# Kernel tuning notes

Hardware: AMD Instinct MI355X
Metric: run time of the kernel (lower is better)

## Reference

```python
import jax, jax.numpy as jnp
import numpy as np

Q, C, D, H, K, B, T = 10000, 200, 64, 64, 4, 512, 200
MAX_DISC = 10.0


def setup_inputs() -> dict:
    key = jax.random.key(0)
    ks = jax.random.split(key, 24)

    def p(k, shape, s=0.05):
        return jax.random.normal(k, shape, jnp.float32) * s

    mid_qd = (D + C) // 2   # 132
    mid_la = (H + C) // 2   # 132
    mid_dc = (D + 1) // 2   # 32
    inp = {
        'E_q': p(ks[0], (Q + 1, D)),
        'E_c': p(ks[1], (C + 1, D)),
        'E_it': p(ks[2], (101, D)),
        'E_ut': p(ks[3], (101, D)),
        'E_nh': p(ks[4], (101, D)),
        'W_fuse': p(ks[5], (D, 3 * D)), 'b_fuse': jnp.zeros((D,), jnp.float32),
        'W_ih': p(ks[6], (3 * H, 5 * D)), 'b_ih': jnp.zeros((3 * H,), jnp.float32),
        'W_hh': p(ks[7], (3 * H, H)), 'b_hh': jnp.zeros((3 * H,), jnp.float32),
        'qd_W1': p(ks[8], (mid_qd, D)), 'qd_b1': jnp.zeros((mid_qd,), jnp.float32),
        'qd_W2': p(ks[9], (C, mid_qd)), 'qd_b2': jnp.zeros((C,), jnp.float32),
        'la_W1': p(ks[10], (mid_la, H)), 'la_b1': jnp.zeros((mid_la,), jnp.float32),
        'la_W2': p(ks[11], (C, mid_la)), 'la_b2': jnp.zeros((C,), jnp.float32),
        'dc_W1': p(ks[12], (mid_dc, D)), 'dc_b1': jnp.zeros((mid_dc,), jnp.float32),
        'dc_W2': p(ks[13], (1, mid_dc)), 'dc_b2': jnp.zeros((1,), jnp.float32),
    }
    inp['question_seq'] = jax.random.randint(ks[14], (B, T), 0, Q + 1, jnp.int32)
    inp['correct_seq'] = jax.random.randint(ks[15], (B, T), 0, 2, jnp.int32)
    inp['interval_time_seq'] = jax.random.randint(ks[16], (B, T), 0, 101, jnp.int32)
    inp['use_time_seq'] = jax.random.randint(ks[17], (B, T), 0, 101, jnp.int32)
    inp['num_hint_seq'] = jax.random.randint(ks[18], (B, T), 0, 101, jnp.int32)
    inp['num_attempt_seq'] = jax.random.randint(ks[19], (B, T), 0, 101, jnp.int32)
    # per-question concept lists + padding mask (first nc entries valid)
    q2c = jax.random.randint(ks[20], (Q + 1, K), 0, C, jnp.int32)
    nc = jax.random.randint(ks[21], (Q + 1,), 1, K + 1, jnp.int32)
    mask = (jnp.arange(K, dtype=jnp.int32)[None, :] < nc[:, None]).astype(jnp.int32)
    inp['q2c_table'] = q2c
    inp['q2c_mask'] = mask
    rows = jnp.arange(Q + 1)[:, None]
    inp['Q_table'] = jnp.zeros((Q + 1, C), jnp.float32).at[rows, q2c].max(mask.astype(jnp.float32))
    return inp


def mlp2(x, W1, b1, W2, b2):
    # MLP4Proj, num_layer=2, eval-mode dropout == identity
    return jax.nn.relu(x @ W1.T + b1) @ W2.T + b2


def gru(x, W_ih, b_ih, W_hh, b_hh):
    # torch nn.GRU, 1 layer, batch_first; gate order r,z,n
    xp = jnp.einsum('btd,gd->btg', x, W_ih) + b_ih  # [B,T,3H]

    def step(h, xp_t):
        gh = h @ W_hh.T + b_hh
        xr, xz, xn = jnp.split(xp_t, 3, axis=-1)
        hr, hz, hn = jnp.split(gh, 3, axis=-1)
        r = jax.nn.sigmoid(xr + hr)
        z = jax.nn.sigmoid(xz + hz)
        n = jnp.tanh(xn + r * hn)
        h_new = (1.0 - z) * n + z * h
        return h_new, h_new

    h0 = jnp.zeros((x.shape[0], W_hh.shape[1]), x.dtype)
    _, hs = jax.lax.scan(step, h0, jnp.swapaxes(xp, 0, 1))
    return jnp.swapaxes(hs, 0, 1)  # [B,T,H]


def reference(E_q, E_c, E_it, E_ut, E_nh, W_fuse, b_fuse, W_ih, b_ih, W_hh, b_hh,
              qd_W1, qd_b1, qd_W2, qd_b2, la_W1, la_b1, la_W2, la_b2,
              dc_W1, dc_b1, dc_W2, dc_b2, Q_table,
              question_seq, correct_seq, interval_time_seq, use_time_seq,
              num_hint_seq, num_attempt_seq, q2c_table, q2c_mask):
    qe = E_q[question_seq]                                   # [B,T,D]
    # get_concept_emb: difficulty-weighted concept fusion
    qd = jax.nn.sigmoid(mlp2(qe, qd_W1, qd_b1, qd_W2, qd_b2))  # [B,T,C]
    qc_idx = q2c_table[question_seq]                          # [B,T,K]
    msk = q2c_mask[question_seq].astype(qe.dtype)             # [B,T,K]
    rel = jnp.take_along_axis(qd, qc_idx, axis=2) * msk       # [B,T,K]
    srel = rel.sum(-1, keepdims=True) + 1e-6
    ce = (rel[..., None] * E_c[qc_idx]).sum(-2) / srel        # [B,T,D]
    corr = jnp.broadcast_to(correct_seq[..., None].astype(qe.dtype), qe.shape)
    inter = jnp.concatenate([qe, ce, corr], axis=-1)          # [B,T,3D]
    # aux-info fusion (source bug: num_attempt also uses embed_num_hint)
    ut_nh_na = jnp.concatenate([E_ut[use_time_seq], E_nh[num_hint_seq], E_nh[num_attempt_seq]], axis=-1)
    fuse = ut_nh_na @ W_fuse.T + b_fuse                       # [B,T,D]
    x = jnp.concatenate([inter, E_it[interval_time_seq], fuse], axis=-1)  # [B,T,5D]
    latent = gru(x, W_ih, b_ih, W_hh, b_hh)                   # [B,T,H]
    # predict_score on shifted slices
    lat, qe2, qs2 = latent[:, :-1], qe[:, 1:], question_seq[:, 1:]
    ua = jax.nn.sigmoid(mlp2(lat, la_W1, la_b1, la_W2, la_b2))       # [B,T-1,C]
    disc = jax.nn.sigmoid(mlp2(qe2, dc_W1, dc_b1, dc_W2, dc_b2)) * MAX_DISC  # [B,T-1,1]
    qd2 = jax.nn.sigmoid(mlp2(qe2, qd_W1, qd_b1, qd_W2, qd_b2))      # [B,T-1,C]
    Qt = Q_table[qs2]                                                # [B,T-1,C]
    ua_m = ua * Qt
    qd_m = qd2 * Qt
    sw = qd_m.sum(-1, keepdims=True) + 1e-6
    y = disc * (ua_m - qd_m) / sw
    return jax.nn.sigmoid(y.sum(-1))                                 # [B,T-1]
```

## Files before the change

kernel.cpp:

```cpp
#include <hip/hip_runtime.h>
#include <hip/hip_fp16.h>

constexpr int QN  = 10001;
constexpr int BB  = 512;
constexpr int TT  = 200;
constexpr int QPB = 32;

__device__ __forceinline__ float sigm(float x) { return 1.f / (1.f + __expf(-x)); }
__device__ __forceinline__ float tanh_fast(float x) { return 1.f - 2.f / (1.f + __expf(2.f * x)); }

__device__ __forceinline__ unsigned packh_rtne(float lo, float hi) {
    return ((unsigned)__half_as_ushort(__float2half(hi)) << 16) |
            (unsigned)__half_as_ushort(__float2half(lo));
}

typedef _Float16 half2_t __attribute__((ext_vector_type(2)));
typedef float f4v __attribute__((ext_vector_type(4)));
__device__ __forceinline__ half2_t u2h(unsigned u) {
    union { unsigned u; half2_t h; } x; x.u = u; return x.h;
}

#if __has_builtin(__builtin_amdgcn_fdot2)
__device__ __forceinline__ float fdot2u(unsigned wu, unsigned hu, float acc) {
    return __builtin_amdgcn_fdot2(u2h(wu), u2h(hu), acc, false);
}
#else
__device__ __forceinline__ float fdot2u(unsigned wu, unsigned hu, float acc) {
    float wlo = __half2float(__ushort_as_half((unsigned short)(wu & 0xffffu)));
    float whi = __half2float(__ushort_as_half((unsigned short)(wu >> 16)));
    float hlo = __half2float(__ushort_as_half((unsigned short)(hu & 0xffffu)));
    float hhi = __half2float(__ushort_as_half((unsigned short)(hu >> 16)));
    return acc + wlo * hlo + whi * hhi;
}
#endif

__global__ void k_tables(const float* __restrict__ E_c, const float* __restrict__ E_it,
                         const float* __restrict__ E_ut, const float* __restrict__ E_nh,
                         const float* __restrict__ W_fuse, const float* __restrict__ b_fuse,
                         const float* __restrict__ W_ih, const float* __restrict__ b_ih,
                         float* __restrict__ T_c, float* __restrict__ T_it,
                         float* __restrict__ T_ut, float* __restrict__ T_nh, float* __restrict__ T_na,
                         float* __restrict__ bias0, float* __restrict__ Vcorr)
{
    int blk = blockIdx.x, j = threadIdx.x;
    __shared__ float s_e[64];
    __shared__ float s_t[64];
    const int ilv = (j & 63) * 3 + (j >> 6);

    if (blk < 201) {
        if (j < 64) s_e[j] = E_c[blk * 64 + j];
        __syncthreads();
        float a = 0.f;
        #pragma unroll
        for (int k = 0; k < 64; k++) a += W_ih[j * 320 + 64 + k] * s_e[k];
        T_c[blk * 192 + j] = a;
    } else if (blk < 302) {
        int r = blk - 201;
        if (j < 64) s_e[j] = E_it[r * 64 + j];
        __syncthreads();
        float a = 0.f;
        #pragma unroll
        for (int k = 0; k < 64; k++) a += W_ih[j * 320 + 192 + k] * s_e[k];
        T_it[r * 192 + ilv] = a;
    } else if (blk < 605) {
        int which = (blk - 302) / 101;
        int r     = (blk - 302) % 101;
        const float* E = (which == 0) ? E_ut : E_nh;
        int fofs = which * 64;
        if (j < 64) s_e[j] = E[r * 64 + j];
        __syncthreads();
        if (j < 64) {
            float a = 0.f;
            #pragma unroll
            for (int d = 0; d < 64; d++) a += W_fuse[j * 192 + fofs + d] * s_e[d];
            s_t[j] = a;
        }
        __syncthreads();
        float a = 0.f;
        #pragma unroll
        for (int e = 0; e < 64; e++) a += W_ih[j * 320 + 256 + e] * s_t[e];
        float* outp = (which == 0) ? T_ut : ((which == 1) ? T_nh : T_na);
        outp[r * 192 + ilv] = a;
    } else {
        float a = b_ih[j];
        #pragma unroll
        for (int e = 0; e < 64; e++) a += W_ih[j * 320 + 256 + e] * b_fuse[e];
        bias0[j] = a;
        float v = 0.f;
        #pragma unroll
        for (int k = 0; k < 64; k++) v += W_ih[j * 320 + 128 + k];
        Vcorr[j] = v;
    }
}

__global__ void __launch_bounds__(192) k_perq(
    const float* __restrict__ E_q, const float* __restrict__ W_ih,
    const float* __restrict__ qd_W1, const float* __restrict__ qd_b1,
    const float* __restrict__ qd_W2, const float* __restrict__ qd_b2,
    const float* __restrict__ dc_W1, const float* __restrict__ dc_b1,
    const float* __restrict__ dc_W2, const float* __restrict__ dc_b2,
    const int* __restrict__ q2c, const int* __restrict__ q2cm,
    const float* __restrict__ T_c,
    float* __restrict__ Xq, float* __restrict__ disc,
    float* __restrict__ qds, float* __restrict__ wdk)
{
    __shared__ float s_wbuf[192 * 66];
    __shared__ float s_qe[QPB][64];
    __shared__ float s_wq[QPB][4];
    __shared__ int   s_cq[QPB][4];
    __shared__ float s_hidw[3][136];

    const int tid = threadIdx.x, w = tid >> 6, l = tid & 63;
    const int q0 = blockIdx.x * QPB;

    for (int i = tid; i < 132 * 64; i += 192)
        s_wbuf[(i >> 6) * 66 + (i & 63)] = qd_W1[i];
    for (int i = tid; i < 32 * 64; i += 192)
        s_wbuf[(132 + (i >> 6)) * 66 + (i & 63)] = dc_W1[i];
    for (int i = tid; i < QPB * 64; i += 192) {
        int qq = i >> 6, q = q0 + qq;
        s_qe[qq][i & 63] = E_q[(q < QN ? q : 0) * 64 + (i & 63)];
    }
    __syncthreads();

    for (int qq = w; qq < QPB; qq += 3) {
        int q = q0 + qq;
        bool valid = q < QN;
        int qc = valid ? q : 0;
        int cc[4], mm[4];
        #pragma unroll
        for (int k = 0; k < 4; k++) { cc[k] = q2c[qc * 4 + k]; mm[k] = q2cm[qc * 4 + k]; }

        float qe[64];
        #pragma unroll
        for (int k4 = 0; k4 < 16; k4++) {
            float4 v = *(const float4*)(&s_qe[qq][k4 * 4]);
            qe[4 * k4] = v.x; qe[4 * k4 + 1] = v.y; qe[4 * k4 + 2] = v.z; qe[4 * k4 + 3] = v.w;
        }

        auto rowdot = [&](int r) {
            const float* wr = s_wbuf + r * 66;
            float a = 0.f;
            #pragma unroll
            for (int jj = 0; jj < 32; jj++) {
                float2 ww = *(const float2*)(wr + 2 * jj);
                a += ww.x * qe[2 * jj] + ww.y * qe[2 * jj + 1];
            }
            return a;
        };

        s_hidw[w][l]      = fmaxf(rowdot(l)      + qd_b1[l],      0.f);
        s_hidw[w][64 + l] = fmaxf(rowdot(64 + l) + qd_b1[64 + l], 0.f);
        if (l < 4)
            s_hidw[w][128 + l] = fmaxf(rowdot(128 + l) + qd_b1[128 + l], 0.f);
        float dch = 0.f;
        if (l < 32) dch = fmaxf(rowdot(132 + l) + dc_b1[l], 0.f);

        int g = l >> 4, li = l & 15;
        int c = cc[g];
        float acc = 0.f;
        #pragma unroll
        for (int i = 0; i < 9; i++) {
            int m = li + 16 * i;
            if (m < 132) acc += qd_W2[c * 132 + m] * s_hidw[w][m];
        }
        acc += __shfl_xor(acc, 1); acc += __shfl_xor(acc, 2);
        acc += __shfl_xor(acc, 4); acc += __shfl_xor(acc, 8);
        float r0 = __shfl(acc, 0), r1 = __shfl(acc, 16);
        float r2 = __shfl(acc, 32), r3 = __shfl(acc, 48);

        float raw[4] = { sigm(r0 + qd_b2[cc[0]]), sigm(r1 + qd_b2[cc[1]]),
                         sigm(r2 + qd_b2[cc[2]]), sigm(r3 + qd_b2[cc[3]]) };
        float rel[4];
        #pragma unroll
        for (int k = 0; k < 4; k++) rel[k] = raw[k] * (float)mm[k];
        float sr = rel[0] + rel[1] + rel[2] + rel[3] + 1e-6f;

        float qsum = 0.f, wdv[4];
        #pragma unroll
        for (int k = 0; k < 4; k++) {
            float wd = 0.f;
            if (mm[k]) {
                bool dup = false;
                for (int jj = 0; jj < k; jj++)
                    if (mm[jj] && cc[jj] == cc[k]) dup = true;
                if (!dup) { wd = 1.f; qsum += raw[k]; }
            }
            wdv[k] = wd;
        }
        if (l < 4) { s_wq[qq][l] = rel[l] / sr; s_cq[qq][l] = cc[l]; }
        if (valid) {
            if (l < 4) wdk[q * 4 + l] = wdv[l];
            if (l == 0) qds[q] = qsum;
        }

        float dv = (l < 32) ? dch * dc_W2[l] : 0.f;
        dv += __shfl_xor(dv, 1);  dv += __shfl_xor(dv, 2);
        dv += __shfl_xor(dv, 4);  dv += __shfl_xor(dv, 8);
        dv += __shfl_xor(dv, 16);
        if (valid && l == 0) disc[q] = sigm(dv + dc_b2[0]) * 10.f;
    }

    __syncthreads();
    for (int i = tid; i < 192 * 64; i += 192) {
        int r = i >> 6, k = i & 63;
        s_wbuf[r * 66 + k] = W_ih[r * 320 + k];
    }
    __syncthreads();

    for (int qq = w; qq < QPB; qq += 3) {
        int q = q0 + qq;
        if (q >= QN) continue;

        float qe[64];
        #pragma unroll
        for (int k4 = 0; k4 < 16; k4++) {
            float4 v = *(const float4*)(&s_qe[qq][k4 * 4]);
            qe[4 * k4] = v.x; qe[4 * k4 + 1] = v.y; qe[4 * k4 + 2] = v.z; qe[4 * k4 + 3] = v.w;
        }
        float wq[4]; int cq[4];
        #pragma unroll
        for (int k = 0; k < 4; k++) { wq[k] = s_wq[qq][k]; cq[k] = s_cq[qq][k]; }

        #pragma unroll
        for (int rr = 0; rr < 3; rr++) {
            int row = rr * 64 + l;
            const float* wr = s_wbuf + row * 66;
            float a = 0.f;
            #pragma unroll
            for (int jj = 0; jj < 32; jj++) {
                float2 ww = *(const float2*)(wr + 2 * jj);
                a += ww.x * qe[2 * jj] + ww.y * qe[2 * jj + 1];
            }
            #pragma unroll
            for (int k = 0; k < 4; k++) a += wq[k] * T_c[cq[k] * 192 + row];
            Xq[q * 192 + l * 3 + rr] = a;
        }
    }
}

__global__ void
__launch_bounds__(64)
__attribute__((amdgpu_waves_per_eu(1, 1)))
k_gru(
    const float* __restrict__ W_hh, const float* __restrict__ b_hh,
    const float* __restrict__ XqI, const float* __restrict__ TitI, const float* __restrict__ TutI,
    const float* __restrict__ TnhI, const float* __restrict__ TnaI,
    const float* __restrict__ b0, const float* __restrict__ vc,
    const int* __restrict__ qseq, const int* __restrict__ cseq, const int* __restrict__ itseq,
    const int* __restrict__ utseq, const int* __restrict__ nhseq, const int* __restrict__ naseq,
    float* __restrict__ latent)
{
    const int j = threadIdx.x, b = blockIdx.x;
    const int j3 = 3 * j;

    __shared__ unsigned s_hp[32];
    __shared__ int s_ix[6 * TT];

    const int base = b * TT;
    for (int i = j; i < TT; i += 64) {
        s_ix[i]          = qseq[base + i];
        s_ix[TT + i]     = cseq[base + i];
        s_ix[2 * TT + i] = itseq[base + i];
        s_ix[3 * TT + i] = utseq[base + i];
        s_ix[4 * TT + i] = nhseq[base + i];
        s_ix[5 * TT + i] = naseq[base + i];
    }

    unsigned wr[32], wz[32], wn[32];
    {
        const float4* p0 = (const float4*)(W_hh + j * 64);
        const float4* p1 = (const float4*)(W_hh + (64 + j) * 64);
        const float4* p2 = (const float4*)(W_hh + (128 + j) * 64);
        #pragma unroll
        for (int k = 0; k < 16; k++) {
            float4 a = p0[k], bq = p1[k], c = p2[k];
            wr[2 * k] = packh_rtne(a.x, a.y);  wr[2 * k + 1] = packh_rtne(a.z, a.w);
            wz[2 * k] = packh_rtne(bq.x, bq.y); wz[2 * k + 1] = packh_rtne(bq.z, bq.w);
            wn[2 * k] = packh_rtne(c.x, c.y);  wn[2 * k + 1] = packh_rtne(c.z, c.w);
        }
    }
    #pragma unroll
    for (int k = 0; k < 32; k++)
        asm volatile("" : "+v"(wr[k]), "+v"(wz[k]), "+v"(wn[k]));

    const float bhr = b_hh[j], bhz = b_hh[64 + j], bhn = b_hh[128 + j];
    const float b0r = b0[j],   b0z = b0[64 + j],   b0n = b0[128 + j];
    const float vcr = vc[j],   vcz = vc[64 + j],   vcn = vc[128 + j];

    if (j < 32) s_hp[j] = 0u;
    float hj = 0.f;

    f4v A0, A1, A2, A3, A4;  float cA;
    f4v B0, B1, B2, B3, B4;  float cB;
    f4v C0, C1, C2, C3, C4;  float cC;
    f4v D0, D1, D2, D3, D4;  float cD;

#define GISSUE(P, CC, tt) { \
        int q_ = s_ix[tt], c_ = s_ix[TT + tt], it_ = s_ix[2 * TT + tt]; \
        int ut_ = s_ix[3 * TT + tt], nh_ = s_ix[4 * TT + tt], na_ = s_ix[5 * TT + tt]; \
        CC = (float)c_; \
        asm volatile("global_load_dwordx4 %0, %1, off" : "=v"(P##0) : "v"(XqI  + q_  * 192 + j3)); \
        asm volatile("global_load_dwordx4 %0, %1, off" : "=v"(P##1) : "v"(TitI + it_ * 192 + j3)); \
        asm volatile("global_load_dwordx4 %0, %1, off" : "=v"(P##2) : "v"(TutI + ut_ * 192 + j3)); \
        asm volatile("global_load_dwordx4 %0, %1, off" : "=v"(P##3) : "v"(TnhI + nh_ * 192 + j3)); \
        asm volatile("global_load_dwordx4 %0, %1, off" : "=v"(P##4) : "v"(TnaI + na_ * 192 + j3)); \
    }

#define STEP(P, CC, tcur, WN, REF) { \
        asm volatile("s_waitcnt vmcnt(" WN ")" ::: "memory"); \
        float xr = b0r + CC * vcr + ((((P##0).x + (P##1).x) + ((P##2).x + (P##3).x)) + (P##4).x); \
        float xz = b0z + CC * vcz + ((((P##0).y + (P##1).y) + ((P##2).y + (P##3).y)) + (P##4).y); \
        float xn = b0n + CC * vcn + ((((P##0).z + (P##1).z) + ((P##2).z + (P##3).z)) + (P##4).z); \
        asm volatile("" :: "v"((P##0).w), "v"((P##1).w), "v"((P##2).w), "v"((P##3).w), "v"((P##4).w)); \
        if (REF) GISSUE(P, CC, (tcur) + 4); \
        float ar0 = 0.f, ar1 = 0.f, ar2 = 0.f, ar3 = 0.f; \
        float az0 = 0.f, az1 = 0.f, az2 = 0.f, az3 = 0.f; \
        float an0 = 0.f, an1 = 0.f, an2 = 0.f, an3 = 0.f; \
        const uint4* hp4 = (const uint4*)s_hp; \
        _Pragma("unroll") \
        for (int k4 = 0; k4 < 8; k4++) { \
            uint4 hh = hp4[k4]; \
            ar0 = fdot2u(wr[4 * k4 + 0], hh.x, ar0); \
            ar1 = fdot2u(wr[4 * k4 + 1], hh.y, ar1); \
            ar2 = fdot2u(wr[4 * k4 + 2], hh.z, ar2); \
            ar3 = fdot2u(wr[4 * k4 + 3], hh.w, ar3); \
            az0 = fdot2u(wz[4 * k4 + 0], hh.x, az0); \
            az1 = fdot2u(wz[4 * k4 + 1], hh.y, az1); \
            az2 = fdot2u(wz[4 * k4 + 2], hh.z, az2); \
            az3 = fdot2u(wz[4 * k4 + 3], hh.w, az3); \
            an0 = fdot2u(wn[4 * k4 + 0], hh.x, an0); \
            an1 = fdot2u(wn[4 * k4 + 1], hh.y, an1); \
            an2 = fdot2u(wn[4 * k4 + 2], hh.z, an2); \
            an3 = fdot2u(wn[4 * k4 + 3], hh.w, an3); \
        } \
        float ar = ((ar0 + ar1) + (ar2 + ar3)) + bhr; \
        float az = ((az0 + az1) + (az2 + az3)) + bhz; \
        float an = ((an0 + an1) + (an2 + an3)) + bhn; \
        float r = sigm(xr + ar); \
        float z = sigm(xz + az); \
        float n = tanh_fast(xn + r * an); \
        hj = (1.f - z) * n + z * hj; \
        latent[(size_t)(base + (tcur)) * 64 + j] = hj; \
        float hnb = __shfl_xor(hj, 1); \
        unsigned pk = (j & 1) ? packh_rtne(hnb, hj) : packh_rtne(hj, hnb); \
        if (!(j & 1)) s_hp[j >> 1] = pk; \
    }

    GISSUE(A, cA, 0);
    GISSUE(B, cB, 1);
    GISSUE(C, cC, 2);
    GISSUE(D, cD, 3);

    for (int t = 0; t < TT - 4; t += 4) {
        STEP(A, cA, t,     "15", 1);
        STEP(B, cB, t + 1, "15", 1);
        STEP(C, cC, t + 2, "15", 1);
        STEP(D, cD, t + 3, "15", 1);
    }
    STEP(A, cA, TT - 4, "15", 0);
    STEP(B, cB, TT - 3, "10", 0);
    STEP(C, cC, TT - 2, "5",  0);
    STEP(D, cD, TT - 1, "0",  0);
#undef STEP
#undef GISSUE
}

__global__ void __launch_bounds__(256) k_final(
    const float* __restrict__ latent, const int* __restrict__ qseq,
    const float* __restrict__ la_W1, const float* __restrict__ la_b1,
    const float* __restrict__ la_W2, const float* __restrict__ la_b2,
    const int* __restrict__ q2c,
    const float* __restrict__ disc, const float* __restrict__ qds,
    const float* __restrict__ wdk, float* __restrict__ out)
{
    __shared__ unsigned short s_w2[200 * 132];
    __shared__ float s_b2[200];

    const int tid = threadIdx.x;
    for (int i = tid; i < 200 * 132; i += 256)
        s_w2[i] = __half_as_ushort(__float2half(la_W2[i]));
    for (int i = tid; i < 200; i += 256) s_b2[i] = la_b2[i];
    __syncthreads();

    int o = blockIdx.x * blockDim.x + tid;
    if (o >= BB * (TT - 1)) return;
    int b = o / (TT - 1), t = o - b * (TT - 1);

    const float* lat = latent + (size_t)(b * TT + t) * 64;
    float l[64];
    #pragma unroll
    for (int k4 = 0; k4 < 16; k4++) {
        float4 v = ((const float4*)lat)[k4];
        l[k4 * 4] = v.x; l[k4 * 4 + 1] = v.y; l[k4 * 4 + 2] = v.z; l[k4 * 4 + 3] = v.w;
    }

    int q = qseq[b * TT + t + 1];
    int c0 = q2c[q * 4], c1 = q2c[q * 4 + 1], c2 = q2c[q * 4 + 2], c3 = q2c[q * 4 + 3];
    const unsigned short* w0p = s_w2 + c0 * 132;
    const unsigned short* w1p = s_w2 + c1 * 132;
    const unsigned short* w2p = s_w2 + c2 * 132;
    const unsigned short* w3p = s_w2 + c3 * 132;

    float u0 = 0.f, u1 = 0.f, u2 = 0.f, u3 = 0.f;
    for (int m = 0; m < 132; m++) {
        float a = la_b1[m];
        const float* w = la_W1 + m * 64;
        #pragma unroll
        for (int k = 0; k < 64; k++) a += w[k] * l[k];
        float hm = fmaxf(a, 0.f);
        u0 += __half2float(__ushort_as_half(w0p[m])) * hm;
        u1 += __half2float(__ushort_as_half(w1p[m])) * hm;
        u2 += __half2float(__ushort_as_half(w2p[m])) * hm;
        u3 += __half2float(__ushort_as_half(w3p[m])) * hm;
    }

    float w0 = wdk[q * 4], w1 = wdk[q * 4 + 1], w2 = wdk[q * 4 + 2], w3 = wdk[q * 4 + 3];
    float us = w0 * sigm(u0 + s_b2[c0]) + w1 * sigm(u1 + s_b2[c1])
             + w2 * sigm(u2 + s_b2[c2]) + w3 * sigm(u3 + s_b2[c3]);
    float qs = qds[q];
    float y = disc[q] * (us - qs) / (qs + 1e-6f);
    out[o] = sigm(y);
}

extern "C" void kernel_launch(void* const* d_in, const int* in_sizes, int n_in,
                              void* d_out, int out_size, void* d_ws, size_t ws_size,
                              hipStream_t stream)
{
    const float* E_q    = (const float*)d_in[0];
    const float* E_c    = (const float*)d_in[1];
    const float* E_it   = (const float*)d_in[2];
    const float* E_ut   = (const float*)d_in[3];
    const float* E_nh   = (const float*)d_in[4];
    const float* W_fuse = (const float*)d_in[5];
    const float* b_fuse = (const float*)d_in[6];
    const float* W_ih   = (const float*)d_in[7];
    const float* b_ih   = (const float*)d_in[8];
    const float* W_hh   = (const float*)d_in[9];
    const float* b_hh   = (const float*)d_in[10];
    const float* qd_W1  = (const float*)d_in[11];
    const float* qd_b1  = (const float*)d_in[12];
    const float* qd_W2  = (const float*)d_in[13];
    const float* qd_b2  = (const float*)d_in[14];
    const float* la_W1  = (const float*)d_in[15];
    const float* la_b1  = (const float*)d_in[16];
    const float* la_W2  = (const float*)d_in[17];
    const float* la_b2  = (const float*)d_in[18];
    const float* dc_W1  = (const float*)d_in[19];
    const float* dc_b1  = (const float*)d_in[20];
    const float* dc_W2  = (const float*)d_in[21];
    const float* dc_b2  = (const float*)d_in[22];

    int off = (in_sizes[23] == QN * 200) ? 1 : 0;
    const int* qseq  = (const int*)d_in[23 + off];
    const int* cseq  = (const int*)d_in[24 + off];
    const int* itseq = (const int*)d_in[25 + off];
    const int* utseq = (const int*)d_in[26 + off];
    const int* nhseq = (const int*)d_in[27 + off];
    const int* naseq = (const int*)d_in[28 + off];
    const int* q2c   = (const int*)d_in[29 + off];
    const int* q2cm  = (const int*)d_in[30 + off];

    float* ws = (float*)d_ws;
    size_t o = 0;
    float* T_c  = ws + o; o += (size_t)201 * 192 + 4;
    float* Tit  = ws + o; o += (size_t)101 * 192 + 4;
    float* Tut  = ws + o; o += (size_t)101 * 192 + 4;
    float* Tnh  = ws + o; o += (size_t)101 * 192 + 4;
    float* Tna  = ws + o; o += (size_t)101 * 192 + 4;
    float* b0   = ws + o; o += 192;
    float* vc   = ws + o; o += 192;
    float* Xq   = ws + o; o += (size_t)QN * 192 + 4;
    float* disc = ws + o; o += QN;
    float* qds  = ws + o; o += QN;
    float* wdk  = ws + o; o += (size_t)QN * 4;
    float* latent = ws + o; o += (size_t)BB * TT * 64;

    float* outp = (float*)d_out;

    k_tables<<<606, 192, 0, stream>>>(E_c, E_it, E_ut, E_nh, W_fuse, b_fuse, W_ih, b_ih,
                                      T_c, Tit, Tut, Tnh, Tna, b0, vc);
    k_perq<<<(QN + QPB - 1) / QPB, 192, 0, stream>>>(E_q, W_ih, qd_W1, qd_b1, qd_W2, qd_b2,
                                                     dc_W1, dc_b1, dc_W2, dc_b2, q2c, q2cm, T_c,
                                                     Xq, disc, qds, wdk);
    k_gru<<<BB, 64, 0, stream>>>(W_hh, b_hh, Xq, Tit, Tut, Tnh, Tna, b0, vc,
                                 qseq, cseq, itseq, utseq, nhseq, naseq, latent);
    k_final<<<(BB * (TT - 1) + 255) / 256, 256, 0, stream>>>(latent, qseq, la_W1, la_b1,
                                                             la_W2, la_b2, q2c, disc, qds, wdk, outp);
}
```

Baseline: 324.6 us.

## Restructure final scoring kernel to wave-per-token with register-resident fp16 W1

The final prediction kernel now assigns one wavefront per token instead of one thread per token. Each lane holds two rows of la_W1 as packed fp16 in registers and computes hidden units with fdot2, then reduces the concept logits with cross-lane shuffles. The kernel runs as a persistent grid of 512 blocks. The intent is to remove the per-thread serial 132x64 fp32 matvec and its heavy global/L1 weight traffic. In exchange it adds fp16 precision loss in the first layer, per-token shuffle reductions, and higher register pressure. The GRU kernel also gets a VGPR attribute.

```diff
diff --git a/kernel.cpp b/kernel.cpp
--- a/kernel.cpp
+++ b/kernel.cpp
@@ -12,6 +12,9 @@
 __device__ __forceinline__ unsigned packh_rtne(float lo, float hi) {
     return ((unsigned)__half_as_ushort(__float2half(hi)) << 16) |
             (unsigned)__half_as_ushort(__float2half(lo));
+}
+__device__ __forceinline__ float h2f_lo(unsigned short u) {
+    return __half2float(__ushort_as_half(u));
 }
 
 typedef _Float16 half2_t __attribute__((ext_vector_type(2)));
@@ -241,7 +244,7 @@
 
 __global__ void
 __launch_bounds__(64)
-__attribute__((amdgpu_waves_per_eu(1, 1)))
+__attribute__((amdgpu_num_vgpr(256), amdgpu_waves_per_eu(1, 1)))
 k_gru(
     const float* __restrict__ W_hh, const float* __restrict__ b_hh,
     const float* __restrict__ XqI, const float* __restrict__ TitI, const float* __restrict__ TutI,
@@ -366,7 +369,7 @@
 #undef GISSUE
 }
 
-__global__ void __launch_bounds__(256) k_final(
+__global__ void __launch_bounds__(256, 1) k_final(
     const float* __restrict__ latent, const int* __restrict__ qseq,
     const float* __restrict__ la_W1, const float* __restrict__ la_b1,
     const float* __restrict__ la_W2, const float* __restrict__ la_b2,
@@ -374,53 +377,122 @@
     const float* __restrict__ disc, const float* __restrict__ qds,
     const float* __restrict__ wdk, float* __restrict__ out)
 {
-    __shared__ unsigned short s_w2[200 * 132];
-    __shared__ float s_b2[200];
-
-    const int tid = threadIdx.x;
-    for (int i = tid; i < 200 * 132; i += 256)
-        s_w2[i] = __half_as_ushort(__float2half(la_W2[i]));
-    for (int i = tid; i < 200; i += 256) s_b2[i] = la_b2[i];
+    __shared__ float s_rawf[13600];
+    __shared__ unsigned s_w1t[4][33];
+    __shared__ unsigned s_lat[4][36];
+
+    const int tid = threadIdx.x, wv = tid >> 6, l = tid & 63;
+
+    for (int i = tid; i < 132 * 64; i += 256)
+        s_rawf[(i >> 6) * 67 + (i & 63)] = la_W1[i];
     __syncthreads();
 
-    int o = blockIdx.x * blockDim.x + tid;
-    if (o >= BB * (TT - 1)) return;
-    int b = o / (TT - 1), t = o - b * (TT - 1);
-
-    const float* lat = latent + (size_t)(b * TT + t) * 64;
-    float l[64];
+    unsigned w1a[32], w1b[32];
+    {
+        const float* r0 = s_rawf + l * 67;
+        const float* r1 = s_rawf + (64 + l) * 67;
+        #pragma unroll
+        for (int k = 0; k < 32; k++) {
+            w1a[k] = packh_rtne(r0[2 * k], r0[2 * k + 1]);
+            w1b[k] = packh_rtne(r1[2 * k], r1[2 * k + 1]);
+        }
+    }
+    for (int i = tid; i < 4 * 32; i += 256) {
+        int row = i >> 5, k = i & 31;
+        s_w1t[row][k] = packh_rtne(s_rawf[(128 + row) * 67 + 2 * k],
+                                   s_rawf[(128 + row) * 67 + 2 * k + 1]);
+    }
     #pragma unroll
-    for (int k4 = 0; k4 < 16; k4++) {
-        float4 v = ((const float4*)lat)[k4];
-        l[k4 * 4] = v.x; l[k4 * 4 + 1] = v.y; l[k4 * 4 + 2] = v.z; l[k4 * 4 + 3] = v.w;
-    }
-
-    int q = qseq[b * TT + t + 1];
-    int c0 = q2c[q * 4], c1 = q2c[q * 4 + 1], c2 = q2c[q * 4 + 2], c3 = q2c[q * 4 + 3];
-    const unsigned short* w0p = s_w2 + c0 * 132;
-    const unsigned short* w1p = s_w2 + c1 * 132;
-    const unsigned short* w2p = s_w2 + c2 * 132;
-    const unsigned short* w3p = s_w2 + c3 * 132;
-
-    float u0 = 0.f, u1 = 0.f, u2 = 0.f, u3 = 0.f;
-    for (int m = 0; m < 132; m++) {
-        float a = la_b1[m];
-        const float* w = la_W1 + m * 64;
-        #pragma unroll
-        for (int k = 0; k < 64; k++) a += w[k] * l[k];
-        float hm = fmaxf(a, 0.f);
-        u0 += __half2float(__ushort_as_half(w0p[m])) * hm;
-        u1 += __half2float(__ushort_as_half(w1p[m])) * hm;
-        u2 += __half2float(__ushort_as_half(w2p[m])) * hm;
-        u3 += __half2float(__ushort_as_half(w3p[m])) * hm;
-    }
-
-    float w0 = wdk[q * 4], w1 = wdk[q * 4 + 1], w2 = wdk[q * 4 + 2], w3 = wdk[q * 4 + 3];
-    float us = w0 * sigm(u0 + s_b2[c0]) + w1 * sigm(u1 + s_b2[c1])
-             + w2 * sigm(u2 + s_b2[c2]) + w3 * sigm(u3 + s_b2[c3]);
-    float qs = qds[q];
-    float y = disc[q] * (us - qs) / (qs + 1e-6f);
-    out[o] = sigm(y);
+    for (int k = 0; k < 32; k++)
+        asm volatile("" : "+v"(w1a[k]), "+v"(w1b[k]));
+    __syncthreads();
+
+    unsigned short* w2v = (unsigned short*)s_rawf;
+    for (int i = tid; i < 200 * 132; i += 256) {
+        int c = i / 132, m = i - c * 132;
+        w2v[c * 136 + m] = __half_as_ushort(__float2half(la_W2[i]));
+    }
+    __syncthreads();
+
+    const float bl0 = la_b1[l], bl1 = la_b1[64 + l];
+    const float bl2 = (l < 4) ? la_b1[128 + l] : 0.f;
+
+    const int nTok = BB * (TT - 1);
+    const int waveId = blockIdx.x * 4 + wv;
+    const int nWaves = gridDim.x * 4;
+
+    for (int tok = waveId; tok < nTok; tok += nWaves) {
+        int b = tok / (TT - 1), t = tok - b * (TT - 1);
+
+        float lv = latent[(size_t)(b * TT + t) * 64 + l];
+        float lo = __shfl_xor(lv, 1);
+        if (!(l & 1)) s_lat[wv][l >> 1] = packh_rtne(lv, lo);
+        asm volatile("s_waitcnt lgkmcnt(0)" ::: "memory");
+
+        uint4 L[8];
+        {
+            const uint4* lp = (const uint4*)s_lat[wv];
+            #pragma unroll
+            for (int k4 = 0; k4 < 8; k4++) L[k4] = lp[k4];
+        }
+
+        float a0 = 0.f, a1 = 0.f, a2 = 0.f, a3 = 0.f;
+        float c0a = 0.f, c1a = 0.f, c2a = 0.f, c3a = 0.f;
+        #pragma unroll
+        for (int k4 = 0; k4 < 8; k4++) {
+            uint4 hh = L[k4];
+            a0  = fdot2u(w1a[4 * k4 + 0], hh.x, a0);
+            a1  = fdot2u(w1a[4 * k4 + 1], hh.y, a1);
+            a2  = fdot2u(w1a[4 * k4 + 2], hh.z, a2);
+            a3  = fdot2u(w1a[4 * k4 + 3], hh.w, a3);
+            c0a = fdot2u(w1b[4 * k4 + 0], hh.x, c0a);
+            c1a = fdot2u(w1b[4 * k4 + 1], hh.y, c1a);
+            c2a = fdot2u(w1b[4 * k4 + 2], hh.z, c2a);
+            c3a = fdot2u(w1b[4 * k4 + 3], hh.w, c3a);
+        }
+        float hm0 = fmaxf(((a0 + a1) + (a2 + a3)) + bl0, 0.f);
+        float hm1 = fmaxf(((c0a + c1a) + (c2a + c3a)) + bl1, 0.f);
+
+        float hm2 = 0.f;
+        if (l < 4) {
+            float h = 0.f;
+            const unsigned* wt = s_w1t[l];
+            const unsigned* lu = (const unsigned*)s_lat[wv];
+            #pragma unroll
+            for (int k = 0; k < 32; k++) h = fdot2u(wt[k], lu[k], h);
+            hm2 = fmaxf(h + bl2, 0.f);
+        }
+
+        int q  = qseq[b * TT + t + 1];
+        int c0 = q2c[q * 4], c1 = q2c[q * 4 + 1], c2 = q2c[q * 4 + 2], c3 = q2c[q * 4 + 3];
+
+        float u0 = h2f_lo(w2v[c0 * 136 + l]) * hm0 + h2f_lo(w2v[c0 * 136 + 64 + l]) * hm1;
+        float u1 = h2f_lo(w2v[c1 * 136 + l]) * hm0 + h2f_lo(w2v[c1 * 136 + 64 + l]) * hm1;
+        float u2 = h2f_lo(w2v[c2 * 136 + l]) * hm0 + h2f_lo(w2v[c2 * 136 + 64 + l]) * hm1;
+        float u3 = h2f_lo(w2v[c3 * 136 + l]) * hm0 + h2f_lo(w2v[c3 * 136 + 64 + l]) * hm1;
+        if (l < 4) {
+            u0 += h2f_lo(w2v[c0 * 136 + 128 + l]) * hm2;
+            u1 += h2f_lo(w2v[c1 * 136 + 128 + l]) * hm2;
+            u2 += h2f_lo(w2v[c2 * 136 + 128 + l]) * hm2;
+            u3 += h2f_lo(w2v[c3 * 136 + 128 + l]) * hm2;
+        }
+        #pragma unroll
+        for (int off = 32; off; off >>= 1) {
+            u0 += __shfl_xor(u0, off);
+            u1 += __shfl_xor(u1, off);
+            u2 += __shfl_xor(u2, off);
+            u3 += __shfl_xor(u3, off);
+        }
+
+        if (l == 0) {
+            float w0 = wdk[q * 4], w1 = wdk[q * 4 + 1], w2w = wdk[q * 4 + 2], w3 = wdk[q * 4 + 3];
+            float us = w0 * sigm(u0 + la_b2[c0]) + w1 * sigm(u1 + la_b2[c1])
+                     + w2w * sigm(u2 + la_b2[c2]) + w3 * sigm(u3 + la_b2[c3]);
+            float qs = qds[q];
+            float y = disc[q] * (us - qs) / (qs + 1e-6f);
+            out[tok] = sigm(y);
+        }
+    }
 }
 
 extern "C" void kernel_launch(void* const* d_in, const int* in_sizes, int n_in,
@@ -485,6 +557,6 @@
                                                      Xq, disc, qds, wdk);
     k_gru<<<BB, 64, 0, stream>>>(W_hh, b_hh, Xq, Tit, Tut, Tnh, Tna, b0, vc,
                                  qseq, cseq, itseq, utseq, nhseq, naseq, latent);
-    k_final<<<(BB * (TT - 1) + 255) / 256, 256, 0, stream>>>(latent, qseq, la_W1, la_b1,
-                                                             la_W2, la_b2, q2c, disc, qds, wdk, outp);
-}
+    k_final<<<512, 256, 0, stream>>>(latent, qseq, la_W1, la_b1,
+                                     la_W2, la_b2, q2c, disc, qds, wdk, outp);
+}
```

After: 366.7 us. 1.13x slower.

## Stage GRU input-gate gathers through LDS via global_load_lds with padded rows

Applied to the files above, without the earlier changes.

Pads the per-index input-projection tables from 3 to 4 floats per hidden unit so each row is 16-byte aligned. The GRU kernel then gathers them with direct global-to-LDS loads into a four-slot shared ring buffer instead of asm loads into registers. This is meant to free the 20 prefetch vector registers held across steps and keep the four-step-ahead gather pipeline. In exchange it adds an LDS read and wait per step, changes the vmcnt thresholds, and uses a third more table memory and bandwidth.

```diff
diff --git a/kernel.cpp b/kernel.cpp
--- a/kernel.cpp
+++ b/kernel.cpp
@@ -33,6 +33,12 @@
     return acc + wlo * hlo + whi * hhi;
 }
 #endif
+
+typedef const __attribute__((address_space(1))) void cgv_t;
+typedef __attribute__((address_space(3))) void lv_t;
+__device__ __forceinline__ void glds16(const float* g, float* l) {
+    __builtin_amdgcn_global_load_lds((cgv_t*)g, (lv_t*)l, 16, 0, 0);
+}
 
 __global__ void k_tables(const float* __restrict__ E_c, const float* __restrict__ E_it,
                          const float* __restrict__ E_ut, const float* __restrict__ E_nh,
@@ -45,7 +51,7 @@
     int blk = blockIdx.x, j = threadIdx.x;
     __shared__ float s_e[64];
     __shared__ float s_t[64];
-    const int ilv = (j & 63) * 3 + (j >> 6);
+    const int ilv4 = (j & 63) * 4 + (j >> 6);
 
     if (blk < 201) {
         if (j < 64) s_e[j] = E_c[blk * 64 + j];
@@ -61,7 +67,7 @@
         float a = 0.f;
         #pragma unroll
         for (int k = 0; k < 64; k++) a += W_ih[j * 320 + 192 + k] * s_e[k];
-        T_it[r * 192 + ilv] = a;
+        T_it[r * 256 + ilv4] = a;
     } else if (blk < 605) {
         int which = (blk - 302) / 101;
         int r     = (blk - 302) % 101;
@@ -80,7 +86,7 @@
         #pragma unroll
         for (int e = 0; e < 64; e++) a += W_ih[j * 320 + 256 + e] * s_t[e];
         float* outp = (which == 0) ? T_ut : ((which == 1) ? T_nh : T_na);
-        outp[r * 192 + ilv] = a;
+        outp[r * 256 + ilv4] = a;
     } else {
         float a = b_ih[j];
         #pragma unroll
@@ -234,7 +240,7 @@
             }
             #pragma unroll
             for (int k = 0; k < 4; k++) a += wq[k] * T_c[cq[k] * 192 + row];
-            Xq[q * 192 + l * 3 + rr] = a;
+            Xq[q * 256 + l * 4 + rr] = a;
         }
     }
 }
@@ -252,8 +258,9 @@
     float* __restrict__ latent)
 {
     const int j = threadIdx.x, b = blockIdx.x;
-    const int j3 = 3 * j;
-
+    const int j4 = 4 * j;
+
+    __shared__ float s_gb[4][5][64][4];
     __shared__ unsigned s_hp[32];
     __shared__ int s_ix[6 * TT];
 
@@ -291,29 +298,31 @@
     if (j < 32) s_hp[j] = 0u;
     float hj = 0.f;
 
-    f4v A0, A1, A2, A3, A4;  float cA;
-    f4v B0, B1, B2, B3, B4;  float cB;
-    f4v C0, C1, C2, C3, C4;  float cC;
-    f4v D0, D1, D2, D3, D4;  float cD;
-
-#define GISSUE(P, CC, tt) { \
+    float cA, cB, cC, cD;
+
+#define GISSUE(S, CCV, tt) { \
         int q_ = s_ix[tt], c_ = s_ix[TT + tt], it_ = s_ix[2 * TT + tt]; \
         int ut_ = s_ix[3 * TT + tt], nh_ = s_ix[4 * TT + tt], na_ = s_ix[5 * TT + tt]; \
-        CC = (float)c_; \
-        asm volatile("global_load_dwordx4 %0, %1, off" : "=v"(P##0) : "v"(XqI  + q_  * 192 + j3)); \
-        asm volatile("global_load_dwordx4 %0, %1, off" : "=v"(P##1) : "v"(TitI + it_ * 192 + j3)); \
-        asm volatile("global_load_dwordx4 %0, %1, off" : "=v"(P##2) : "v"(TutI + ut_ * 192 + j3)); \
-        asm volatile("global_load_dwordx4 %0, %1, off" : "=v"(P##3) : "v"(TnhI + nh_ * 192 + j3)); \
-        asm volatile("global_load_dwordx4 %0, %1, off" : "=v"(P##4) : "v"(TnaI + na_ * 192 + j3)); \
-    }
-
-#define STEP(P, CC, tcur, WN, REF) { \
+        CCV = (float)c_; \
+        glds16(XqI  + q_  * 256 + j4, &s_gb[S][0][0][0]); \
+        glds16(TitI + it_ * 256 + j4, &s_gb[S][1][0][0]); \
+        glds16(TutI + ut_ * 256 + j4, &s_gb[S][2][0][0]); \
+        glds16(TnhI + nh_ * 256 + j4, &s_gb[S][3][0][0]); \
+        glds16(TnaI + na_ * 256 + j4, &s_gb[S][4][0][0]); \
+    }
+
+#define STEP(S, CCV, tcur, WN, REF) { \
         asm volatile("s_waitcnt vmcnt(" WN ")" ::: "memory"); \
-        float xr = b0r + CC * vcr + ((((P##0).x + (P##1).x) + ((P##2).x + (P##3).x)) + (P##4).x); \
-        float xz = b0z + CC * vcz + ((((P##0).y + (P##1).y) + ((P##2).y + (P##3).y)) + (P##4).y); \
-        float xn = b0n + CC * vcn + ((((P##0).z + (P##1).z) + ((P##2).z + (P##3).z)) + (P##4).z); \
-        asm volatile("" :: "v"((P##0).w), "v"((P##1).w), "v"((P##2).w), "v"((P##3).w), "v"((P##4).w)); \
-        if (REF) GISSUE(P, CC, (tcur) + 4); \
+        f4v g0 = *(const f4v*)&s_gb[S][0][j][0]; \
+        f4v g1 = *(const f4v*)&s_gb[S][1][j][0]; \
+        f4v g2 = *(const f4v*)&s_gb[S][2][j][0]; \
+        f4v g3 = *(const f4v*)&s_gb[S][3][j][0]; \
+        f4v g4 = *(const f4v*)&s_gb[S][4][j][0]; \
+        asm volatile("s_waitcnt lgkmcnt(0)" ::: "memory"); \
+        float xr = b0r + CCV * vcr + (((g0.x + g1.x) + (g2.x + g3.x)) + g4.x); \
+        float xz = b0z + CCV * vcz + (((g0.y + g1.y) + (g2.y + g3.y)) + g4.y); \
+        float xn = b0n + CCV * vcn + (((g0.z + g1.z) + (g2.z + g3.z)) + g4.z); \
+        if (REF) GISSUE(S, CCV, (tcur) + 4); \
         float ar0 = 0.f, ar1 = 0.f, ar2 = 0.f, ar3 = 0.f; \
         float az0 = 0.f, az1 = 0.f, az2 = 0.f, az3 = 0.f; \
         float an0 = 0.f, an1 = 0.f, an2 = 0.f, an3 = 0.f; \
@@ -347,21 +356,26 @@
         if (!(j & 1)) s_hp[j >> 1] = pk; \
     }
 
-    GISSUE(A, cA, 0);
-    GISSUE(B, cB, 1);
-    GISSUE(C, cC, 2);
-    GISSUE(D, cD, 3);
-
-    for (int t = 0; t < TT - 4; t += 4) {
-        STEP(A, cA, t,     "15", 1);
-        STEP(B, cB, t + 1, "15", 1);
-        STEP(C, cC, t + 2, "15", 1);
-        STEP(D, cD, t + 3, "15", 1);
-    }
-    STEP(A, cA, TT - 4, "15", 0);
-    STEP(B, cB, TT - 3, "10", 0);
-    STEP(C, cC, TT - 2, "5",  0);
-    STEP(D, cD, TT - 1, "0",  0);
+    GISSUE(0, cA, 0);
+    GISSUE(1, cB, 1);
+    GISSUE(2, cC, 2);
+    GISSUE(3, cD, 3);
+
+    STEP(0, cA, 0, "15", 1);
+    STEP(1, cB, 1, "16", 1);
+    STEP(2, cC, 2, "17", 1);
+    STEP(3, cD, 3, "18", 1);
+
+    for (int t = 4; t <= TT - 8; t += 4) {
+        STEP(0, cA, t,     "18", 1);
+        STEP(1, cB, t + 1, "18", 1);
+        STEP(2, cC, t + 2, "18", 1);
+        STEP(3, cD, t + 3, "18", 1);
+    }
+    STEP(0, cA, TT - 4, "18", 0);
+    STEP(1, cB, TT - 3, "12", 0);
+    STEP(2, cC, TT - 2, "6",  0);
+    STEP(3, cD, TT - 1, "0",  0);
 #undef STEP
 #undef GISSUE
 }
@@ -463,14 +477,14 @@
 
     float* ws = (float*)d_ws;
     size_t o = 0;
-    float* T_c  = ws + o; o += (size_t)201 * 192 + 4;
-    float* Tit  = ws + o; o += (size_t)101 * 192 + 4;
-    float* Tut  = ws + o; o += (size_t)101 * 192 + 4;
-    float* Tnh  = ws + o; o += (size_t)101 * 192 + 4;
-    float* Tna  = ws + o; o += (size_t)101 * 192 + 4;
+    float* T_c  = ws + o; o += (size_t)201 * 192;
+    float* Tit  = ws + o; o += (size_t)101 * 256;
+    float* Tut  = ws + o; o += (size_t)101 * 256;
+    float* Tnh  = ws + o; o += (size_t)101 * 256;
+    float* Tna  = ws + o; o += (size_t)101 * 256;
     float* b0   = ws + o; o += 192;
     float* vc   = ws + o; o += 192;
-    float* Xq   = ws + o; o += (size_t)QN * 192 + 4;
+    float* Xq   = ws + o; o += (size_t)QN * 256;
     float* disc = ws + o; o += QN;
     float* qds  = ws + o; o += QN;
     float* wdk  = ws + o; o += (size_t)QN * 4;
```

After: 328.4 us. About the same (+1.2%).
